# Performance work log

Measured on AMD Instinct MI355X. Metric: run time of the kernel, lower is better.

## Reference

```python
import jax, jax.numpy as jnp
import numpy as np

D_MODEL, D_INNER, D_STATE, DT_RANK, D_CONV = 768, 1536, 16, 48, 4
B, L = 2, 2048


def setup_inputs() -> dict:
    key = jax.random.key(0)
    ks = jax.random.split(key, 8)
    s = 0.02
    return {
        "x": jax.random.normal(ks[0], (B, L, D_MODEL), jnp.float32),
        "norm_w": jnp.ones((D_MODEL,), jnp.float32),
        "in_proj_w": jax.random.normal(ks[1], (2 * D_INNER, D_MODEL), jnp.float32) * s,
        "conv_w": jax.random.normal(ks[2], (D_INNER, 1, D_CONV), jnp.float32) * s,
        "conv_b": jnp.zeros((D_INNER,), jnp.float32),
        "x_proj_w": jax.random.normal(ks[3], (DT_RANK + 2 * D_STATE, D_INNER), jnp.float32) * s,
        "dt_proj_w": jax.random.normal(ks[4], (D_INNER, DT_RANK), jnp.float32) * s,
        "dt_proj_b": jax.random.normal(ks[5], (D_INNER,), jnp.float32) * s,
        "A_log": jnp.broadcast_to(jnp.log(jnp.arange(1, D_STATE + 1, dtype=jnp.float32)), (D_INNER, D_STATE)).copy(),
        "D": jnp.ones((D_INNER,), jnp.float32),
        "out_proj_w": jax.random.normal(ks[6], (D_MODEL, D_INNER), jnp.float32) * s,
    }


def _mamba_block(x, norm_w, in_proj_w, conv_w, conv_b, x_proj_w,
                 dt_proj_w, dt_proj_b, A_log, D, out_proj_w):
    residual = x
    # RMSNorm
    h = x * jax.lax.rsqrt(jnp.mean(x * x, axis=-1, keepdims=True) + 1e-5) * norm_w
    # in_proj -> chunk into (hs, gate)
    xz = jnp.einsum('bld,ed->ble', h, in_proj_w)          # [B,L,2*Di]
    xh, z = jnp.split(xz, 2, axis=-1)                     # each [B,L,Di]
    # causal depthwise conv1d (kernel D_CONV) + SiLU
    xt = jnp.transpose(xh, (0, 2, 1))                     # [B,Di,L]
    xt = jnp.pad(xt, ((0, 0), (0, 0), (D_CONV - 1, 0)))
    xc = jax.lax.conv_general_dilated(xt, conv_w, (1,), 'VALID',
                                      feature_group_count=D_INNER)
    xc = jax.nn.silu(xc + conv_b[None, :, None])
    xc = jnp.transpose(xc, (0, 2, 1))                     # [B,L,Di]
    # x_proj -> (dt, B, C)
    proj = jnp.einsum('bld,ed->ble', xc, x_proj_w)        # [B,L,dt_rank+2N]
    dt, Bm, Cm = jnp.split(proj, [DT_RANK, DT_RANK + D_STATE], axis=-1)
    delta = jax.nn.softplus(jnp.einsum('blr,dr->bld', dt, dt_proj_w) + dt_proj_b)  # [B,L,Di]
    A = -jnp.exp(A_log)                                   # [Di,N]
    dA = jnp.exp(delta[..., None] * A)                    # [B,L,Di,N]
    dBx = delta[..., None] * Bm[:, :, None, :] * xc[..., None]  # [B,L,Di,N]
    # selective scan over the sequence axis
    def step(hst, inp):
        dA_t, dBx_t, C_t = inp                            # [B,Di,N],[B,Di,N],[B,N]
        hst = dA_t * hst + dBx_t
        y = jnp.einsum('bdn,bn->bd', hst, C_t)
        return hst, y
    h0 = jnp.zeros((x.shape[0], D_INNER, D_STATE), x.dtype)
    _, ys = jax.lax.scan(step, h0, (jnp.moveaxis(dA, 1, 0),
                                    jnp.moveaxis(dBx, 1, 0),
                                    jnp.moveaxis(Cm, 1, 0)))
    y = jnp.moveaxis(ys, 0, 1)                            # [B,L,Di]
    y = y + xc * D                                        # skip connection D
    y = y * jax.nn.silu(z)                                # gate
    out = jnp.einsum('bld,ed->ble', y, out_proj_w)        # [B,L,Dm]
    return residual + out, residual


def reference(x, norm_w, in_proj_w, conv_w, conv_b, x_proj_w,
              dt_proj_w, dt_proj_b, A_log, D, out_proj_w):
    return _mamba_block(x, norm_w, in_proj_w, conv_w, conv_b, x_proj_w,
                        dt_proj_w, dt_proj_b, A_log, D, out_proj_w)
```

## Files before the change

kernel.cpp:

```cpp
#include <hip/hip_runtime.h>
#include <cstdint>
#include <cstddef>

typedef __bf16 bf16_t;
typedef __bf16 bf16x8 __attribute__((ext_vector_type(8)));
typedef float  f32x4  __attribute__((ext_vector_type(4)));

#define D_MODEL 768
#define D_INNER 1536
#define D_STATE 16
#define DT_RANK 48
#define NB      2
#define SEQ     2048
#define NTOK    (NB*SEQ)
#define XPROJ_N (DT_RANK + 2*D_STATE)
#define LC      32
#define NCHUNK  (SEQ/LC)
#define XP_KS   4
#define XP_KC   (D_INNER/XP_KS)

#define N_INW (2*D_INNER*D_MODEL)
#define N_XPW (XPROJ_N*D_INNER)
#define N_DTW (D_INNER*DT_RANK)
#define N_OPW (D_MODEL*D_INNER)
#define N_CVT (N_INW+N_XPW+N_DTW+N_OPW)
#define CVT_BLOCKS (N_CVT/1024)

typedef __attribute__((address_space(1))) void gvoid_t;
typedef __attribute__((address_space(3))) void lvoid_t;
__device__ __forceinline__ void g2lds16(const bf16_t* g, bf16_t* l) {
    __builtin_amdgcn_global_load_lds((gvoid_t*)g, (lvoid_t*)l, 16, 0, 0);
}

__global__ __launch_bounds__(256)
void prep_kernel(const float* __restrict__ in_proj_w, bf16_t* __restrict__ w_in,
                 const float* __restrict__ x_proj_w,  bf16_t* __restrict__ w_xp,
                 const float* __restrict__ dt_proj_w, bf16_t* __restrict__ w_dt,
                 const float* __restrict__ out_proj_w,bf16_t* __restrict__ w_op,
                 const float* __restrict__ x, const float* __restrict__ norm_w,
                 bf16_t* __restrict__ h,
                 float* __restrict__ out0, float* __restrict__ out1) {
    const int blk = blockIdx.x;
    const int tid = threadIdx.x;
    if (blk < CVT_BLOCKS) {
        int off = (blk * 256 + tid) * 4;
        const float* s; bf16_t* d;
        if (off < N_INW) { s = in_proj_w + off; d = w_in + off; }
        else if ((off -= N_INW) < N_XPW) { s = x_proj_w + off; d = w_xp + off; }
        else if ((off -= N_XPW) < N_DTW) { s = dt_proj_w + off; d = w_dt + off; }
        else { off -= N_DTW; s = out_proj_w + off; d = w_op + off; }
        float4 v = *(const float4*)s;
        d[0] = (bf16_t)v.x; d[1] = (bf16_t)v.y;
        d[2] = (bf16_t)v.z; d[3] = (bf16_t)v.w;
        return;
    }
    int t = blk - CVT_BLOCKS;
    const float* xr = x + (size_t)t * D_MODEL;
    float v[3];
    float ss = 0.f;
#pragma unroll
    for (int i = 0; i < 3; i++) { v[i] = xr[tid + 256*i]; ss += v[i]*v[i]; }
#pragma unroll
    for (int off = 32; off >= 1; off >>= 1) ss += __shfl_down(ss, off);
    __shared__ float red[4];
    int lane = tid & 63, wv = tid >> 6;
    if (lane == 0) red[wv] = ss;
    __syncthreads();
    float tot = red[0] + red[1] + red[2] + red[3];
    float r = rsqrtf(tot * (1.f/(float)D_MODEL) + 1e-5f);
#pragma unroll
    for (int i = 0; i < 3; i++) {
        size_t idx = (size_t)t*D_MODEL + tid + 256*i;
        h[idx] = (bf16_t)(v[i] * r * norm_w[tid + 256*i]);
        out0[idx] = v[i];
        out1[idx] = v[i];
    }
}

__global__ __launch_bounds__(256)
void gemm_nt128(const bf16_t* __restrict__ A, int lda,
                const bf16_t* __restrict__ B, int ldb,
                bf16_t* __restrict__ C, int ldc, int K) {
    __shared__ __align__(16) bf16_t As[2][128*32];
    __shared__ __align__(16) bf16_t Bs[2][128*32];
    const int tid = threadIdx.x;
    const int wave = tid >> 6, lane = tid & 63;
    const int quad = lane >> 4, l16 = lane & 15;
    const int nbx = gridDim.x, nby = gridDim.y;
    int bid = blockIdx.y * nbx + blockIdx.x;
    const int cpx = (nbx * nby) >> 3;
    bid = (bid & 7) * cpx + (bid >> 3);
    const int m0 = (bid / nby) * 128, n0 = (bid % nby) * 128;
    const int wr = (wave >> 1) * 64, wc = (wave & 1) * 64;

    const int s0 = tid, s1 = tid + 256;
    const int r0 = s0 >> 2, q0 = ((s0 & 3) ^ ((r0 >> 1) & 3)) << 3;
    const int r1 = s1 >> 2, q1 = ((s1 & 3) ^ ((r1 >> 1) & 3)) << 3;

    const bf16_t* Ar0 = A + (size_t)(m0 + r0)*lda + q0;
    const bf16_t* Ar1 = A + (size_t)(m0 + r1)*lda + q1;
    const bf16_t* Br0 = B + (size_t)(n0 + r0)*ldb + q0;
    const bf16_t* Br1 = B + (size_t)(n0 + r1)*ldb + q1;

    f32x4 acc[4][4] = {};
    const int nit = K >> 5;

    g2lds16(Ar0, &As[0][wave*512]);
    g2lds16(Ar1, &As[0][wave*512 + 2048]);
    g2lds16(Br0, &Bs[0][wave*512]);
    g2lds16(Br1, &Bs[0][wave*512 + 2048]);

    for (int it = 0; it < nit; it++) {
        __syncthreads();
        if (it + 1 < nit) {
            int k = (it + 1) << 5;
            int nb = (it + 1) & 1;
            g2lds16(Ar0 + k, &As[nb][wave*512]);
            g2lds16(Ar1 + k, &As[nb][wave*512 + 2048]);
            g2lds16(Br0 + k, &Bs[nb][wave*512]);
            g2lds16(Br1 + k, &Bs[nb][wave*512 + 2048]);
        }
        const int buf = it & 1;
        bf16x8 af[4], bfr[4];
#pragma unroll
        for (int i = 0; i < 4; i++) {
            int rr = wr + i*16 + l16;
            af[i] = *(const bf16x8*)&As[buf][rr*32 + ((quad ^ ((rr >> 1) & 3)) << 3)];
        }
#pragma unroll
        for (int j = 0; j < 4; j++) {
            int rr = wc + j*16 + l16;
            bfr[j] = *(const bf16x8*)&Bs[buf][rr*32 + ((quad ^ ((rr >> 1) & 3)) << 3)];
        }
#pragma unroll
        for (int i = 0; i < 4; i++)
#pragma unroll
            for (int j = 0; j < 4; j++)
                acc[i][j] = __builtin_amdgcn_mfma_f32_16x16x32_bf16(af[i], bfr[j], acc[i][j], 0, 0, 0);
    }

#pragma unroll
    for (int i = 0; i < 4; i++)
#pragma unroll
        for (int j = 0; j < 4; j++) {
            int n = n0 + wc + j*16 + l16;
#pragma unroll
            for (int rr = 0; rr < 4; rr++) {
                int m = m0 + wr + i*16 + quad*4 + rr;
                C[(size_t)m * ldc + n] = (bf16_t)acc[i][j][rr];
            }
        }
}

__global__ __launch_bounds__(256)
void gemm_op(const bf16_t* __restrict__ A, const bf16_t* __restrict__ B,
             float* __restrict__ C) {
    __shared__ __align__(16) bf16_t As[2][128*32];
    __shared__ __align__(16) bf16_t Bs[2][128*32];
    const int tid = threadIdx.x;
    const int wave = tid >> 6, lane = tid & 63;
    const int quad = lane >> 4, l16 = lane & 15;
    const int nbx = gridDim.x, nby = gridDim.y;
    int bid = blockIdx.y * nbx + blockIdx.x;
    const int cpx = (nbx * nby) >> 3;
    bid = (bid & 7) * cpx + (bid >> 3);
    const int m0 = (bid / nby) * 128, n0 = (bid % nby) * 128;
    const int kbase = blockIdx.z * (D_INNER/2);
    const int wr = (wave >> 1) * 64, wc = (wave & 1) * 64;

    const int s0 = tid, s1 = tid + 256;
    const int r0 = s0 >> 2, q0 = ((s0 & 3) ^ ((r0 >> 1) & 3)) << 3;
    const int r1 = s1 >> 2, q1 = ((s1 & 3) ^ ((r1 >> 1) & 3)) << 3;

    const bf16_t* Ar0 = A + (size_t)(m0 + r0)*D_INNER + kbase + q0;
    const bf16_t* Ar1 = A + (size_t)(m0 + r1)*D_INNER + kbase + q1;
    const bf16_t* Br0 = B + (size_t)(n0 + r0)*D_INNER + kbase + q0;
    const bf16_t* Br1 = B + (size_t)(n0 + r1)*D_INNER + kbase + q1;

    f32x4 acc[4][4] = {};
    const int nit = (D_INNER/2) >> 5;

    g2lds16(Ar0, &As[0][wave*512]);
    g2lds16(Ar1, &As[0][wave*512 + 2048]);
    g2lds16(Br0, &Bs[0][wave*512]);
    g2lds16(Br1, &Bs[0][wave*512 + 2048]);

    for (int it = 0; it < nit; it++) {
        __syncthreads();
        if (it + 1 < nit) {
            int k = (it + 1) << 5;
            int nb = (it + 1) & 1;
            g2lds16(Ar0 + k, &As[nb][wave*512]);
            g2lds16(Ar1 + k, &As[nb][wave*512 + 2048]);
            g2lds16(Br0 + k, &Bs[nb][wave*512]);
            g2lds16(Br1 + k, &Bs[nb][wave*512 + 2048]);
        }
        const int buf = it & 1;
        bf16x8 af[4], bfr[4];
#pragma unroll
        for (int i = 0; i < 4; i++) {
            int rr = wr + i*16 + l16;
            af[i] = *(const bf16x8*)&As[buf][rr*32 + ((quad ^ ((rr >> 1) & 3)) << 3)];
        }
#pragma unroll
        for (int j = 0; j < 4; j++) {
            int rr = wc + j*16 + l16;
            bfr[j] = *(const bf16x8*)&Bs[buf][rr*32 + ((quad ^ ((rr >> 1) & 3)) << 3)];
        }
#pragma unroll
        for (int i = 0; i < 4; i++)
#pragma unroll
            for (int j = 0; j < 4; j++)
                acc[i][j] = __builtin_amdgcn_mfma_f32_16x16x32_bf16(af[i], bfr[j], acc[i][j], 0, 0, 0);
    }

#pragma unroll
    for (int i = 0; i < 4; i++)
#pragma unroll
        for (int j = 0; j < 4; j++) {
            int n = n0 + wc + j*16 + l16;
#pragma unroll
            for (int rr = 0; rr < 4; rr++) {
                int m = m0 + wr + i*16 + quad*4 + rr;
                unsafeAtomicAdd(&C[(size_t)m * D_MODEL + n], acc[i][j][rr]);
            }
        }
}

__global__ __launch_bounds__(256)
void gemm_xp(const bf16_t* __restrict__ A, const bf16_t* __restrict__ B,
             float* __restrict__ pbuf) {
    __shared__ __align__(16) bf16_t As[64*32];
    __shared__ __align__(16) bf16_t Bs[64*32];
    const int tid = threadIdx.x;
    const int m0 = blockIdx.x * 64, n0 = blockIdx.y * 64, kbase = blockIdx.z * XP_KC;
    const int r  = tid >> 2, p8 = (tid & 3) << 3;
    const int q8 = (((tid & 3) ^ ((r >> 1) & 3)) << 3);
    const int wave = tid >> 6, lane = tid & 63;
    const int quad = lane >> 4, l16 = lane & 15;

    f32x4 acc[4] = {{0.f,0.f,0.f,0.f},{0.f,0.f,0.f,0.f},
                    {0.f,0.f,0.f,0.f},{0.f,0.f,0.f,0.f}};

    for (int k0 = 0; k0 < XP_KC; k0 += 32) {
        int gk = kbase + k0 + q8;
        uint4 va = *(const uint4*)(A + (size_t)(m0 + r) * D_INNER + gk);
        *(uint4*)&As[r*32 + p8] = va;
        uint4 vb = {0u,0u,0u,0u};
        int nr = n0 + r;
        if (nr < XPROJ_N)
            vb = *(const uint4*)(B + (size_t)nr * D_INNER + gk);
        *(uint4*)&Bs[r*32 + p8] = vb;

        __syncthreads();
        int ra = wave*16 + l16;
        bf16x8 af = *(const bf16x8*)&As[ra*32 + ((quad ^ ((ra >> 1) & 3)) << 3)];
#pragma unroll
        for (int nt = 0; nt < 4; nt++) {
            int rb = nt*16 + l16;
            bf16x8 bfg = *(const bf16x8*)&Bs[rb*32 + ((quad ^ ((rb >> 1) & 3)) << 3)];
            acc[nt] = __builtin_amdgcn_mfma_f32_16x16x32_bf16(af, bfg, acc[nt], 0, 0, 0);
        }
        __syncthreads();
    }

#pragma unroll
    for (int nt = 0; nt < 4; nt++) {
        int n = n0 + nt*16 + l16;
        if (n >= XPROJ_N) continue;
#pragma unroll
        for (int rr = 0; rr < 4; rr++) {
            int m = m0 + wave*16 + quad*4 + rr;
            pbuf[((size_t)blockIdx.z * NTOK + m) * XPROJ_N + n] = acc[nt][rr];
        }
    }
}

__global__ __launch_bounds__(256)
void xp_reduce_kernel(const float* __restrict__ pbuf, bf16_t* __restrict__ proj) {
    int i = blockIdx.x * 256 + threadIdx.x;
    if (i >= NTOK * XPROJ_N) return;
    float s = 0.f;
#pragma unroll
    for (int z = 0; z < XP_KS; z++)
        s += pbuf[(size_t)z * NTOK * XPROJ_N + i];
    proj[i] = (bf16_t)s;
}

__global__ __launch_bounds__(256)
void gemm_dt(const bf16_t* __restrict__ A, const bf16_t* __restrict__ B,
             bf16_t* __restrict__ C, const float* __restrict__ bias) {
    __shared__ __align__(16) bf16_t As[64*32];
    __shared__ __align__(16) bf16_t Bs[64*32];
    const int tid = threadIdx.x;
    const int m0 = blockIdx.x * 64, n0 = blockIdx.y * 64;
    const int r  = tid >> 2, p8 = (tid & 3) << 3;
    const int q8 = (((tid & 3) ^ ((r >> 1) & 3)) << 3);
    const int wave = tid >> 6, lane = tid & 63;
    const int quad = lane >> 4, l16 = lane & 15;

    f32x4 acc[4] = {{0.f,0.f,0.f,0.f},{0.f,0.f,0.f,0.f},
                    {0.f,0.f,0.f,0.f},{0.f,0.f,0.f,0.f}};

    for (int k0 = 0; k0 < DT_RANK; k0 += 32) {
        int gk = k0 + q8;
        uint4 va = {0u,0u,0u,0u};
        if (gk + 8 <= DT_RANK)
            va = *(const uint4*)(A + (size_t)(m0 + r) * XPROJ_N + gk);
        *(uint4*)&As[r*32 + p8] = va;
        uint4 vb = {0u,0u,0u,0u};
        if (gk + 8 <= DT_RANK)
            vb = *(const uint4*)(B + (size_t)(n0 + r) * DT_RANK + gk);
        *(uint4*)&Bs[r*32 + p8] = vb;

        __syncthreads();
        int ra = wave*16 + l16;
        bf16x8 af = *(const bf16x8*)&As[ra*32 + ((quad ^ ((ra >> 1) & 3)) << 3)];
#pragma unroll
        for (int nt = 0; nt < 4; nt++) {
            int rb = nt*16 + l16;
            bf16x8 bfg = *(const bf16x8*)&Bs[rb*32 + ((quad ^ ((rb >> 1) & 3)) << 3)];
            acc[nt] = __builtin_amdgcn_mfma_f32_16x16x32_bf16(af, bfg, acc[nt], 0, 0, 0);
        }
        __syncthreads();
    }

#pragma unroll
    for (int nt = 0; nt < 4; nt++) {
        int n = n0 + nt*16 + l16;
#pragma unroll
        for (int rr = 0; rr < 4; rr++) {
            int m = m0 + wave*16 + quad*4 + rr;
            float u = acc[nt][rr] + bias[n];
            float sp = (u > 20.f) ? u : log1pf(__expf(u));
            C[(size_t)m * D_INNER + n] = (bf16_t)sp;
        }
    }
}

__global__ __launch_bounds__(192)
void conv_silu_kernel(const bf16_t* __restrict__ xz,
                      const float* __restrict__ cw,
                      const float* __restrict__ cb,
                      bf16_t* __restrict__ xc) {
    const int t0 = blockIdx.x * 4;
    const int l0 = t0 & (SEQ - 1);
    const int d = threadIdx.x * 8;

    float cwf[32];
#pragma unroll
    for (int q = 0; q < 8; q++)
        *(float4*)&cwf[q*4] = *(const float4*)&cw[d*4 + q*4];

    float cbv[8];
    *(float4*)&cbv[0] = *(const float4*)&cb[d];
    *(float4*)&cbv[4] = *(const float4*)&cb[d+4];

    bf16x8 rows[7];
#pragma unroll
    for (int r = 0; r < 7; r++) {
        if (l0 - 3 + r >= 0) {
            rows[r] = *(const bf16x8*)&xz[(size_t)(t0 - 3 + r) * (2*D_INNER) + d];
        } else {
#pragma unroll
            for (int i = 0; i < 8; i++) rows[r][i] = (bf16_t)0.f;
        }
    }

#pragma unroll
    for (int tt = 0; tt < 4; tt++) {
        float acc[8];
#pragma unroll
        for (int i = 0; i < 8; i++) acc[i] = cbv[i];
#pragma unroll
        for (int k = 0; k < 4; k++)
#pragma unroll
            for (int i = 0; i < 8; i++)
                acc[i] += (float)rows[tt + k][i] * cwf[i*4 + k];
        bf16x8 o;
#pragma unroll
        for (int i = 0; i < 8; i++) {
            float s = acc[i] / (1.f + __expf(-acc[i]));
            o[i] = (bf16_t)s;
        }
        *(bf16x8*)&xc[(size_t)(t0 + tt) * D_INNER + d] = o;
    }
}

__global__ __launch_bounds__(256)
void scan_part1(const bf16_t* __restrict__ delta,
                const bf16_t* __restrict__ xc,
                const bf16_t* __restrict__ proj,
                const float* __restrict__ A_log,
                float* __restrict__ chunk_h, float* __restrict__ chunk_P) {
    const int tid = threadIdx.x;
    const int d = blockIdx.x * 256 + tid;
    const int c = blockIdx.y;
    const int b = blockIdx.z;
    __shared__ float Bs[LC][D_STATE];
    for (int i = tid; i < LC*D_STATE; i += 256) {
        int l = i >> 4, n = i & 15;
        size_t t = (size_t)b*SEQ + (size_t)c*LC + l;
        Bs[l][n] = (float)proj[t*XPROJ_N + DT_RANK + n];
    }
    __syncthreads();
    float Av2[D_STATE];
#pragma unroll
    for (int n = 0; n < D_STATE; n++)
        Av2[n] = -__expf(A_log[d*D_STATE + n]) * 1.44269504f;
    float s[D_STATE];
#pragma unroll
    for (int n = 0; n < D_STATE; n++) s[n] = 0.f;
    float sdv = 0.f;
    const size_t tbase = (size_t)b*SEQ + (size_t)c*LC;
    for (int l = 0; l < LC; l++) {
        size_t t = tbase + l;
        float dv  = (float)delta[t*D_INNER + d];
        float xcv = (float)xc[t*D_INNER + d];
        float dx = dv * xcv;
        sdv += dv;
#pragma unroll
        for (int n = 0; n < D_STATE; n++) {
            float a = __builtin_amdgcn_exp2f(dv * Av2[n]);
            s[n] = a * s[n] + dx * Bs[l][n];
        }
    }
    size_t base = (((size_t)b*NCHUNK + c)*D_INNER + d)*D_STATE;
#pragma unroll
    for (int n = 0; n < D_STATE; n++) {
        chunk_h[base + n] = s[n];
        chunk_P[base + n] = __builtin_amdgcn_exp2f(Av2[n] * sdv);
    }
}

__global__ __launch_bounds__(256)
void scan_part2(float* __restrict__ chunk_h, const float* __restrict__ chunk_P) {
    int gid = blockIdx.x * 256 + threadIdx.x;
    int b  = gid / (D_INNER * D_STATE);
    int dn = gid - b * (D_INNER * D_STATE);
    const size_t cs = (size_t)D_INNER * D_STATE;
    size_t base = (size_t)b * NCHUNK * cs + dn;
    float H = 0.f;
    float S[8], P[8];
#pragma unroll
    for (int j = 0; j < 8; j++) {
        S[j] = chunk_h[base + (size_t)j * cs];
        P[j] = chunk_P[base + (size_t)j * cs];
    }
    for (int g = 0; g < 8; g++) {
        float S2[8], P2[8];
        if (g < 7) {
#pragma unroll
            for (int j = 0; j < 8; j++) {
                S2[j] = chunk_h[base + (size_t)((g+1)*8 + j) * cs];
                P2[j] = chunk_P[base + (size_t)((g+1)*8 + j) * cs];
            }
        }
#pragma unroll
        for (int j = 0; j < 8; j++) {
            size_t idx = base + (size_t)(g*8 + j) * cs;
            chunk_h[idx] = H;
            H = fmaf(P[j], H, S[j]);
        }
#pragma unroll
        for (int j = 0; j < 8; j++) { S[j] = S2[j]; P[j] = P2[j]; }
    }
}

__global__ __launch_bounds__(256)
void scan_part3(const bf16_t* __restrict__ delta,
                const bf16_t* __restrict__ xc,
                const bf16_t* __restrict__ proj,
                const bf16_t* __restrict__ xz,
                const float* __restrict__ A_log,
                const float* __restrict__ Dw,
                const float* __restrict__ chunk_h,
                bf16_t* __restrict__ y) {
    const int tid = threadIdx.x;
    const int d = blockIdx.x * 256 + tid;
    const int c = blockIdx.y;
    const int b = blockIdx.z;
    __shared__ float Bs[LC][D_STATE];
    __shared__ float Cs[LC][D_STATE];
    for (int i = tid; i < LC*D_STATE; i += 256) {
        int l = i >> 4, n = i & 15;
        size_t t = (size_t)b*SEQ + (size_t)c*LC + l;
        Bs[l][n] = (float)proj[t*XPROJ_N + DT_RANK + n];
        Cs[l][n] = (float)proj[t*XPROJ_N + DT_RANK + D_STATE + n];
    }
    __syncthreads();
    float Av2[D_STATE];
#pragma unroll
    for (int n = 0; n < D_STATE; n++)
        Av2[n] = -__expf(A_log[d*D_STATE + n]) * 1.44269504f;
    const float Dv = Dw[d];
    float s[D_STATE];
    size_t base = (((size_t)b*NCHUNK + c)*D_INNER + d)*D_STATE;
#pragma unroll
    for (int n = 0; n < D_STATE; n++) s[n] = chunk_h[base + n];
    const size_t tbase = (size_t)b*SEQ + (size_t)c*LC;
    for (int l = 0; l < LC; l++) {
        size_t t = tbase + l;
        float dv  = (float)delta[t*D_INNER + d];
        float xcv = (float)xc[t*D_INNER + d];
        float dx = dv * xcv;
        float acc = 0.f;
#pragma unroll
        for (int n = 0; n < D_STATE; n++) {
            float a = __builtin_amdgcn_exp2f(dv * Av2[n]);
            s[n] = a * s[n] + dx * Bs[l][n];
            acc += s[n] * Cs[l][n];
        }
        float zf = (float)xz[t*(2*D_INNER) + D_INNER + d];
        float g = zf / (1.f + __expf(-zf));
        y[t*D_INNER + d] = (bf16_t)((acc + xcv * Dv) * g);
    }
}

extern "C" void kernel_launch(void* const* d_in, const int* in_sizes, int n_in,
                              void* d_out, int out_size, void* d_ws, size_t ws_size,
                              hipStream_t stream) {
    const float* x          = (const float*)d_in[0];
    const float* norm_w     = (const float*)d_in[1];
    const float* in_proj_w  = (const float*)d_in[2];
    const float* conv_w     = (const float*)d_in[3];
    const float* conv_b     = (const float*)d_in[4];
    const float* x_proj_w   = (const float*)d_in[5];
    const float* dt_proj_w  = (const float*)d_in[6];
    const float* dt_proj_b  = (const float*)d_in[7];
    const float* A_log      = (const float*)d_in[8];
    const float* Dw         = (const float*)d_in[9];
    const float* out_proj_w = (const float*)d_in[10];

    float* out0 = (float*)d_out;
    float* out1 = out0 + (size_t)NTOK * D_MODEL;

    const size_t n_chunkst = (size_t)NB*NCHUNK*D_INNER*D_STATE;

    char* ws = (char*)d_ws;
    bf16_t* w_in  = (bf16_t*)ws;  ws += (size_t)N_INW * sizeof(bf16_t);
    bf16_t* w_xp  = (bf16_t*)ws;  ws += (size_t)N_XPW * sizeof(bf16_t);
    bf16_t* w_dt  = (bf16_t*)ws;  ws += (size_t)N_DTW * sizeof(bf16_t);
    bf16_t* w_op  = (bf16_t*)ws;  ws += (size_t)N_OPW * sizeof(bf16_t);
    bf16_t* h     = (bf16_t*)ws;  ws += (size_t)NTOK * D_MODEL   * sizeof(bf16_t);
    bf16_t* xz    = (bf16_t*)ws;  ws += (size_t)NTOK * 2*D_INNER * sizeof(bf16_t);
    bf16_t* xc    = (bf16_t*)ws;  ws += (size_t)NTOK * D_INNER   * sizeof(bf16_t);
    bf16_t* proj  = (bf16_t*)ws;  ws += (size_t)NTOK * XPROJ_N   * sizeof(bf16_t);
    bf16_t* delta = (bf16_t*)ws;  ws += (size_t)NTOK * D_INNER   * sizeof(bf16_t);
    bf16_t* y     = (bf16_t*)ws;  ws += (size_t)NTOK * D_INNER   * sizeof(bf16_t);
    float*  ch    = (float*)ws;   ws += n_chunkst * sizeof(float);
    float*  cP    = (float*)ws;   ws += n_chunkst * sizeof(float);
    float*  xppart= (float*)ws;   ws += (size_t)XP_KS * NTOK * XPROJ_N * sizeof(float);

    prep_kernel<<<CVT_BLOCKS + NTOK, 256, 0, stream>>>(
        in_proj_w, w_in, x_proj_w, w_xp, dt_proj_w, w_dt, out_proj_w, w_op,
        x, norm_w, h, out0, out1);
    gemm_nt128<<<dim3(NTOK/128, (2*D_INNER)/128), 256, 0, stream>>>(
        h, D_MODEL, w_in, D_MODEL, xz, 2*D_INNER, D_MODEL);
    conv_silu_kernel<<<NTOK/4, 192, 0, stream>>>(xz, conv_w, conv_b, xc);
    gemm_xp<<<dim3(NTOK/64, 2, XP_KS), 256, 0, stream>>>(xc, w_xp, xppart);
    xp_reduce_kernel<<<(NTOK*XPROJ_N + 255)/256, 256, 0, stream>>>(xppart, proj);
    gemm_dt<<<dim3(NTOK/64, D_INNER/64), 256, 0, stream>>>(proj, w_dt, delta, dt_proj_b);
    scan_part1<<<dim3(D_INNER/256, NCHUNK, NB), 256, 0, stream>>>(
        delta, xc, proj, A_log, ch, cP);
    scan_part2<<<(int)((size_t)NB*D_INNER*D_STATE/256), 256, 0, stream>>>(ch, cP);
    scan_part3<<<dim3(D_INNER/256, NCHUNK, NB), 256, 0, stream>>>(
        delta, xc, proj, xz, A_log, Dw, ch, y);
    gemm_op<<<dim3(NTOK/128, D_MODEL/128, 2), 256, 0, stream>>>(y, w_op, out0);
}
```

Baseline: 276.1 us.

## Fuse dt_proj GEMM and softplus into scan kernels, atomic-reduce x_proj split-K

The separate delta GEMM kernel is removed. Each scan block now recomputes its 64x256 delta tile with MFMA, applies softplus in shared memory, and reads it from there, so the delta tensor is never written to or read from global memory. The x_proj split-K partials are accumulated with float atomics into a proj buffer that prep_kernel zeroes, which drops the reduce kernel. Chunk length doubles to 64 and conv processes 8 tokens per block. The cost is that delta is computed twice (once in part1, once in part3), shared memory use and register pressure per block grow, and the larger chunks halve the number of scan blocks.

```diff
diff --git a/kernel.cpp b/kernel.cpp
--- a/kernel.cpp
+++ b/kernel.cpp
@@ -14,7 +14,7 @@
 #define SEQ     2048
 #define NTOK    (NB*SEQ)
 #define XPROJ_N (DT_RANK + 2*D_STATE)
-#define LC      32
+#define LC      64
 #define NCHUNK  (SEQ/LC)
 #define XP_KS   4
 #define XP_KC   (D_INNER/XP_KS)
@@ -38,7 +38,7 @@
                  const float* __restrict__ dt_proj_w, bf16_t* __restrict__ w_dt,
                  const float* __restrict__ out_proj_w,bf16_t* __restrict__ w_op,
                  const float* __restrict__ x, const float* __restrict__ norm_w,
-                 bf16_t* __restrict__ h,
+                 bf16_t* __restrict__ h, float* __restrict__ proj,
                  float* __restrict__ out0, float* __restrict__ out1) {
     const int blk = blockIdx.x;
     const int tid = threadIdx.x;
@@ -55,6 +55,7 @@
         return;
     }
     int t = blk - CVT_BLOCKS;
+    if (tid < XPROJ_N) proj[(size_t)t * XPROJ_N + tid] = 0.f;
     const float* xr = x + (size_t)t * D_MODEL;
     float v[3];
     float ss = 0.f;
@@ -229,7 +230,7 @@
 
 __global__ __launch_bounds__(256)
 void gemm_xp(const bf16_t* __restrict__ A, const bf16_t* __restrict__ B,
-             float* __restrict__ pbuf) {
+             float* __restrict__ proj) {
     __shared__ __align__(16) bf16_t As[64*32];
     __shared__ __align__(16) bf16_t Bs[64*32];
     const int tid = threadIdx.x;
@@ -271,69 +272,7 @@
 #pragma unroll
         for (int rr = 0; rr < 4; rr++) {
             int m = m0 + wave*16 + quad*4 + rr;
-            pbuf[((size_t)blockIdx.z * NTOK + m) * XPROJ_N + n] = acc[nt][rr];
-        }
-    }
-}
-
-__global__ __launch_bounds__(256)
-void xp_reduce_kernel(const float* __restrict__ pbuf, bf16_t* __restrict__ proj) {
-    int i = blockIdx.x * 256 + threadIdx.x;
-    if (i >= NTOK * XPROJ_N) return;
-    float s = 0.f;
-#pragma unroll
-    for (int z = 0; z < XP_KS; z++)
-        s += pbuf[(size_t)z * NTOK * XPROJ_N + i];
-    proj[i] = (bf16_t)s;
-}
-
-__global__ __launch_bounds__(256)
-void gemm_dt(const bf16_t* __restrict__ A, const bf16_t* __restrict__ B,
-             bf16_t* __restrict__ C, const float* __restrict__ bias) {
-    __shared__ __align__(16) bf16_t As[64*32];
-    __shared__ __align__(16) bf16_t Bs[64*32];
-    const int tid = threadIdx.x;
-    const int m0 = blockIdx.x * 64, n0 = blockIdx.y * 64;
-    const int r  = tid >> 2, p8 = (tid & 3) << 3;
-    const int q8 = (((tid & 3) ^ ((r >> 1) & 3)) << 3);
-    const int wave = tid >> 6, lane = tid & 63;
-    const int quad = lane >> 4, l16 = lane & 15;
-
-    f32x4 acc[4] = {{0.f,0.f,0.f,0.f},{0.f,0.f,0.f,0.f},
-                    {0.f,0.f,0.f,0.f},{0.f,0.f,0.f,0.f}};
-
-    for (int k0 = 0; k0 < DT_RANK; k0 += 32) {
-        int gk = k0 + q8;
-        uint4 va = {0u,0u,0u,0u};
-        if (gk + 8 <= DT_RANK)
-            va = *(const uint4*)(A + (size_t)(m0 + r) * XPROJ_N + gk);
-        *(uint4*)&As[r*32 + p8] = va;
-        uint4 vb = {0u,0u,0u,0u};
-        if (gk + 8 <= DT_RANK)
-            vb = *(const uint4*)(B + (size_t)(n0 + r) * DT_RANK + gk);
-        *(uint4*)&Bs[r*32 + p8] = vb;
-
-        __syncthreads();
-        int ra = wave*16 + l16;
-        bf16x8 af = *(const bf16x8*)&As[ra*32 + ((quad ^ ((ra >> 1) & 3)) << 3)];
-#pragma unroll
-        for (int nt = 0; nt < 4; nt++) {
-            int rb = nt*16 + l16;
-            bf16x8 bfg = *(const bf16x8*)&Bs[rb*32 + ((quad ^ ((rb >> 1) & 3)) << 3)];
-            acc[nt] = __builtin_amdgcn_mfma_f32_16x16x32_bf16(af, bfg, acc[nt], 0, 0, 0);
-        }
-        __syncthreads();
-    }
-
-#pragma unroll
-    for (int nt = 0; nt < 4; nt++) {
-        int n = n0 + nt*16 + l16;
-#pragma unroll
-        for (int rr = 0; rr < 4; rr++) {
-            int m = m0 + wave*16 + quad*4 + rr;
-            float u = acc[nt][rr] + bias[n];
-            float sp = (u > 20.f) ? u : log1pf(__expf(u));
-            C[(size_t)m * D_INNER + n] = (bf16_t)sp;
+            unsafeAtomicAdd(&proj[(size_t)m * XPROJ_N + n], acc[nt][rr]);
         }
     }
 }
@@ -343,7 +282,7 @@
                       const float* __restrict__ cw,
                       const float* __restrict__ cb,
                       bf16_t* __restrict__ xc) {
-    const int t0 = blockIdx.x * 4;
+    const int t0 = blockIdx.x * 8;
     const int l0 = t0 & (SEQ - 1);
     const int d = threadIdx.x * 8;
 
@@ -356,9 +295,9 @@
     *(float4*)&cbv[0] = *(const float4*)&cb[d];
     *(float4*)&cbv[4] = *(const float4*)&cb[d+4];
 
-    bf16x8 rows[7];
-#pragma unroll
-    for (int r = 0; r < 7; r++) {
+    bf16x8 rows[11];
+#pragma unroll
+    for (int r = 0; r < 11; r++) {
         if (l0 - 3 + r >= 0) {
             rows[r] = *(const bf16x8*)&xz[(size_t)(t0 - 3 + r) * (2*D_INNER) + d];
         } else {
@@ -368,7 +307,7 @@
     }
 
 #pragma unroll
-    for (int tt = 0; tt < 4; tt++) {
+    for (int tt = 0; tt < 8; tt++) {
         float acc[8];
 #pragma unroll
         for (int i = 0; i < 8; i++) acc[i] = cbv[i];
@@ -387,23 +326,102 @@
     }
 }
 
-__global__ __launch_bounds__(256)
-void scan_part1(const bf16_t* __restrict__ delta,
-                const bf16_t* __restrict__ xc,
-                const bf16_t* __restrict__ proj,
+__device__ __forceinline__ void delta_mfma(
+    const float* __restrict__ proj, const bf16_t* __restrict__ w_dt,
+    const float* __restrict__ bias, int bx, size_t tbase, int tid,
+    bf16_t* As , bf16_t* Bs , bf16_t* Ds ) {
+    const int wave = tid >> 6, lane = tid & 63;
+    const int quad = lane >> 4, l16 = lane & 15;
+    const int r  = tid >> 2;
+    const int p8 = (tid & 3) << 3;
+    const int x3 = ((tid & 3) ^ ((r >> 1) & 3)) << 3;
+
+    f32x4 acc[4][4] = {};
+
+#pragma unroll
+    for (int kc = 0; kc < 2; kc++) {
+        const int k0 = kc * 32;
+        {
+            int gk = k0 + x3;
+            bf16x8 v;
+            if (gk < DT_RANK) {
+                const float* src = proj + (tbase + r) * XPROJ_N + gk;
+                float4 f0 = *(const float4*)src;
+                float4 f1 = *(const float4*)(src + 4);
+                v[0]=(bf16_t)f0.x; v[1]=(bf16_t)f0.y; v[2]=(bf16_t)f0.z; v[3]=(bf16_t)f0.w;
+                v[4]=(bf16_t)f1.x; v[5]=(bf16_t)f1.y; v[6]=(bf16_t)f1.z; v[7]=(bf16_t)f1.w;
+            } else {
+#pragma unroll
+                for (int i = 0; i < 8; i++) v[i] = (bf16_t)0.f;
+            }
+            *(bf16x8*)&As[r*32 + p8] = v;
+        }
+#pragma unroll
+        for (int it = 0; it < 4; it++) {
+            int row = r + 64*it;
+            uint4 vb = {0u,0u,0u,0u};
+            if (k0 + x3 < DT_RANK)
+                vb = *(const uint4*)(w_dt + (size_t)(bx*256 + row)*DT_RANK + k0 + x3);
+            *(uint4*)&Bs[row*32 + p8] = vb;
+        }
+        __syncthreads();
+        bf16x8 af[4];
+#pragma unroll
+        for (int mi = 0; mi < 4; mi++) {
+            int rr = mi*16 + l16;
+            af[mi] = *(const bf16x8*)&As[rr*32 + ((quad ^ ((rr >> 1) & 3)) << 3)];
+        }
+#pragma unroll
+        for (int nj = 0; nj < 4; nj++) {
+            int rb = wave*64 + nj*16 + l16;
+            bf16x8 bfr = *(const bf16x8*)&Bs[rb*32 + ((quad ^ ((rb >> 1) & 3)) << 3)];
+#pragma unroll
+            for (int mi = 0; mi < 4; mi++)
+                acc[mi][nj] = __builtin_amdgcn_mfma_f32_16x16x32_bf16(af[mi], bfr, acc[mi][nj], 0, 0, 0);
+        }
+        __syncthreads();
+    }
+#pragma unroll
+    for (int nj = 0; nj < 4; nj++) {
+        int dloc = wave*64 + nj*16 + l16;
+        float b = bias[bx*256 + dloc];
+#pragma unroll
+        for (int mi = 0; mi < 4; mi++) {
+#pragma unroll
+            for (int rr2 = 0; rr2 < 4; rr2++) {
+                int t = mi*16 + quad*4 + rr2;
+                float u = acc[mi][nj][rr2] + b;
+                float sp = (u > 20.f) ? u : log1pf(__expf(u));
+                Ds[t*256 + dloc] = (bf16_t)sp;
+            }
+        }
+    }
+    __syncthreads();
+}
+
+__global__ __launch_bounds__(256)
+void scan_part1(const bf16_t* __restrict__ xc,
+                const float* __restrict__ proj,
+                const bf16_t* __restrict__ w_dt,
+                const float* __restrict__ dt_bias,
                 const float* __restrict__ A_log,
                 float* __restrict__ chunk_h, float* __restrict__ chunk_P) {
+    __shared__ __align__(16) bf16_t uraw[64*256];
+    bf16_t* As = uraw;
+    bf16_t* Bs = uraw + 64*32;
+    bf16_t* Ds = uraw;
+    __shared__ float Bsv[LC][D_STATE];
     const int tid = threadIdx.x;
-    const int d = blockIdx.x * 256 + tid;
-    const int c = blockIdx.y;
-    const int b = blockIdx.z;
-    __shared__ float Bs[LC][D_STATE];
+    const int bx = blockIdx.x;
+    const int c = blockIdx.y, b = blockIdx.z;
+    const size_t tbase = (size_t)b*SEQ + (size_t)c*LC;
     for (int i = tid; i < LC*D_STATE; i += 256) {
         int l = i >> 4, n = i & 15;
-        size_t t = (size_t)b*SEQ + (size_t)c*LC + l;
-        Bs[l][n] = (float)proj[t*XPROJ_N + DT_RANK + n];
-    }
-    __syncthreads();
+        Bsv[l][n] = proj[(tbase + l)*XPROJ_N + DT_RANK + n];
+    }
+    delta_mfma(proj, w_dt, dt_bias, bx, tbase, tid, As, Bs, Ds);
+
+    const int d = bx*256 + tid;
     float Av2[D_STATE];
 #pragma unroll
     for (int n = 0; n < D_STATE; n++)
@@ -412,17 +430,15 @@
 #pragma unroll
     for (int n = 0; n < D_STATE; n++) s[n] = 0.f;
     float sdv = 0.f;
-    const size_t tbase = (size_t)b*SEQ + (size_t)c*LC;
     for (int l = 0; l < LC; l++) {
-        size_t t = tbase + l;
-        float dv  = (float)delta[t*D_INNER + d];
-        float xcv = (float)xc[t*D_INNER + d];
+        float dv  = (float)Ds[l*256 + tid];
+        float xcv = (float)xc[(tbase + l)*D_INNER + d];
         float dx = dv * xcv;
         sdv += dv;
 #pragma unroll
         for (int n = 0; n < D_STATE; n++) {
             float a = __builtin_amdgcn_exp2f(dv * Av2[n]);
-            s[n] = a * s[n] + dx * Bs[l][n];
+            s[n] = a * s[n] + dx * Bsv[l][n];
         }
     }
     size_t base = (((size_t)b*NCHUNK + c)*D_INNER + d)*D_STATE;
@@ -447,9 +463,9 @@
         S[j] = chunk_h[base + (size_t)j * cs];
         P[j] = chunk_P[base + (size_t)j * cs];
     }
-    for (int g = 0; g < 8; g++) {
+    for (int g = 0; g < NCHUNK/8; g++) {
         float S2[8], P2[8];
-        if (g < 7) {
+        if (g < NCHUNK/8 - 1) {
 #pragma unroll
             for (int j = 0; j < 8; j++) {
                 S2[j] = chunk_h[base + (size_t)((g+1)*8 + j) * cs];
@@ -468,27 +484,33 @@
 }
 
 __global__ __launch_bounds__(256)
-void scan_part3(const bf16_t* __restrict__ delta,
-                const bf16_t* __restrict__ xc,
-                const bf16_t* __restrict__ proj,
+void scan_part3(const bf16_t* __restrict__ xc,
+                const float* __restrict__ proj,
+                const bf16_t* __restrict__ w_dt,
+                const float* __restrict__ dt_bias,
                 const bf16_t* __restrict__ xz,
                 const float* __restrict__ A_log,
                 const float* __restrict__ Dw,
                 const float* __restrict__ chunk_h,
                 bf16_t* __restrict__ y) {
+    __shared__ __align__(16) bf16_t uraw[64*256];
+    bf16_t* As = uraw;
+    bf16_t* Bs = uraw + 64*32;
+    bf16_t* Ds = uraw;
+    __shared__ float Bsv[LC][D_STATE];
+    __shared__ float Csv[LC][D_STATE];
     const int tid = threadIdx.x;
-    const int d = blockIdx.x * 256 + tid;
-    const int c = blockIdx.y;
-    const int b = blockIdx.z;
-    __shared__ float Bs[LC][D_STATE];
-    __shared__ float Cs[LC][D_STATE];
+    const int bx = blockIdx.x;
+    const int c = blockIdx.y, b = blockIdx.z;
+    const size_t tbase = (size_t)b*SEQ + (size_t)c*LC;
     for (int i = tid; i < LC*D_STATE; i += 256) {
         int l = i >> 4, n = i & 15;
-        size_t t = (size_t)b*SEQ + (size_t)c*LC + l;
-        Bs[l][n] = (float)proj[t*XPROJ_N + DT_RANK + n];
-        Cs[l][n] = (float)proj[t*XPROJ_N + DT_RANK + D_STATE + n];
-    }
-    __syncthreads();
+        Bsv[l][n] = proj[(tbase + l)*XPROJ_N + DT_RANK + n];
+        Csv[l][n] = proj[(tbase + l)*XPROJ_N + DT_RANK + D_STATE + n];
+    }
+    delta_mfma(proj, w_dt, dt_bias, bx, tbase, tid, As, Bs, Ds);
+
+    const int d = bx*256 + tid;
     float Av2[D_STATE];
 #pragma unroll
     for (int n = 0; n < D_STATE; n++)
@@ -498,18 +520,17 @@
     size_t base = (((size_t)b*NCHUNK + c)*D_INNER + d)*D_STATE;
 #pragma unroll
     for (int n = 0; n < D_STATE; n++) s[n] = chunk_h[base + n];
-    const size_t tbase = (size_t)b*SEQ + (size_t)c*LC;
     for (int l = 0; l < LC; l++) {
         size_t t = tbase + l;
-        float dv  = (float)delta[t*D_INNER + d];
+        float dv  = (float)Ds[l*256 + tid];
         float xcv = (float)xc[t*D_INNER + d];
         float dx = dv * xcv;
         float acc = 0.f;
 #pragma unroll
         for (int n = 0; n < D_STATE; n++) {
             float a = __builtin_amdgcn_exp2f(dv * Av2[n]);
-            s[n] = a * s[n] + dx * Bs[l][n];
-            acc += s[n] * Cs[l][n];
+            s[n] = a * s[n] + dx * Bsv[l][n];
+            acc += s[n] * Csv[l][n];
         }
         float zf = (float)xz[t*(2*D_INNER) + D_INNER + d];
         float g = zf / (1.f + __expf(-zf));
@@ -545,26 +566,22 @@
     bf16_t* h     = (bf16_t*)ws;  ws += (size_t)NTOK * D_MODEL   * sizeof(bf16_t);
     bf16_t* xz    = (bf16_t*)ws;  ws += (size_t)NTOK * 2*D_INNER * sizeof(bf16_t);
     bf16_t* xc    = (bf16_t*)ws;  ws += (size_t)NTOK * D_INNER   * sizeof(bf16_t);
-    bf16_t* proj  = (bf16_t*)ws;  ws += (size_t)NTOK * XPROJ_N   * sizeof(bf16_t);
-    bf16_t* delta = (bf16_t*)ws;  ws += (size_t)NTOK * D_INNER   * sizeof(bf16_t);
     bf16_t* y     = (bf16_t*)ws;  ws += (size_t)NTOK * D_INNER   * sizeof(bf16_t);
+    float*  proj  = (float*)ws;   ws += (size_t)NTOK * XPROJ_N   * sizeof(float);
     float*  ch    = (float*)ws;   ws += n_chunkst * sizeof(float);
     float*  cP    = (float*)ws;   ws += n_chunkst * sizeof(float);
-    float*  xppart= (float*)ws;   ws += (size_t)XP_KS * NTOK * XPROJ_N * sizeof(float);
 
     prep_kernel<<<CVT_BLOCKS + NTOK, 256, 0, stream>>>(
         in_proj_w, w_in, x_proj_w, w_xp, dt_proj_w, w_dt, out_proj_w, w_op,
-        x, norm_w, h, out0, out1);
+        x, norm_w, h, proj, out0, out1);
     gemm_nt128<<<dim3(NTOK/128, (2*D_INNER)/128), 256, 0, stream>>>(
         h, D_MODEL, w_in, D_MODEL, xz, 2*D_INNER, D_MODEL);
-    conv_silu_kernel<<<NTOK/4, 192, 0, stream>>>(xz, conv_w, conv_b, xc);
-    gemm_xp<<<dim3(NTOK/64, 2, XP_KS), 256, 0, stream>>>(xc, w_xp, xppart);
-    xp_reduce_kernel<<<(NTOK*XPROJ_N + 255)/256, 256, 0, stream>>>(xppart, proj);
-    gemm_dt<<<dim3(NTOK/64, D_INNER/64), 256, 0, stream>>>(proj, w_dt, delta, dt_proj_b);
+    conv_silu_kernel<<<NTOK/8, 192, 0, stream>>>(xz, conv_w, conv_b, xc);
+    gemm_xp<<<dim3(NTOK/64, 2, XP_KS), 256, 0, stream>>>(xc, w_xp, proj);
     scan_part1<<<dim3(D_INNER/256, NCHUNK, NB), 256, 0, stream>>>(
-        delta, xc, proj, A_log, ch, cP);
+        xc, proj, w_dt, dt_proj_b, A_log, ch, cP);
     scan_part2<<<(int)((size_t)NB*D_INNER*D_STATE/256), 256, 0, stream>>>(ch, cP);
     scan_part3<<<dim3(D_INNER/256, NCHUNK, NB), 256, 0, stream>>>(
-        delta, xc, proj, xz, A_log, Dw, ch, y);
+        xc, proj, w_dt, dt_proj_b, xz, A_log, Dw, ch, y);
     gemm_op<<<dim3(NTOK/128, D_MODEL/128, 2), 256, 0, stream>>>(y, w_op, out0);
 }
```

Result: slower. 316.4 us (+14.6%).
